# Performance work log

Measured on AMD Instinct MI355X. Metric: run time of the kernel, lower is better.

## Reference

```python
import jax, jax.numpy as jnp
import numpy as np

N_NODES = 100000
N_EDGES = 1600000
D_IN = 128
D_HID = 128
D_OUT = 64


def setup_inputs() -> dict:
    key = jax.random.key(0)
    ks = jax.random.split(key, 8)
    x = jax.random.normal(ks[0], (N_NODES, D_IN), dtype=jnp.float32)
    edge_index = jax.random.randint(ks[1], (2, N_EDGES), 0, N_NODES, dtype=jnp.int64)
    s = 1.0 / np.sqrt(D_IN)
    W1l = jax.random.uniform(ks[2], (D_IN, D_HID), minval=-s, maxval=s, dtype=jnp.float32)
    W1r = jax.random.uniform(ks[3], (D_IN, D_HID), minval=-s, maxval=s, dtype=jnp.float32)
    b1 = jnp.zeros((D_HID,), dtype=jnp.float32)
    s2 = 1.0 / np.sqrt(D_HID)
    W2l = jax.random.uniform(ks[4], (D_HID, D_OUT), minval=-s2, maxval=s2, dtype=jnp.float32)
    W2r = jax.random.uniform(ks[5], (D_HID, D_OUT), minval=-s2, maxval=s2, dtype=jnp.float32)
    b2 = jnp.zeros((D_OUT,), dtype=jnp.float32)
    return {"x": x, "edge_index": edge_index, "drpt": 0,
            "W1l": W1l, "W1r": W1r, "b1": b1,
            "W2l": W2l, "W2r": W2r, "b2": b2}


def _mean_aggregate(x, src, dst, n_nodes):
    # gather source features along edges, scatter-mean to destinations
    gathered = x[src]                                   # [E, d]
    summed = jax.ops.segment_sum(gathered, dst, num_segments=n_nodes)  # [N, d]
    deg = jax.ops.segment_sum(jnp.ones((src.shape[0],), x.dtype), dst,
                              num_segments=n_nodes)     # [N]
    return summed / jnp.maximum(deg, 1.0)[:, None]


def _sage_conv(x, src, dst, Wl, Wr, b):
    # PyG SAGEConv (mean): out = agg @ Wl + b + x @ Wr
    agg = _mean_aggregate(x, src, dst, x.shape[0])
    return agg @ Wl + b + x @ Wr


def reference(x, edge_index, drpt, W1l, W1r, b1, W2l, W2r, b2):
    src, dst = edge_index[0], edge_index[1]
    h = _sage_conv(x, src, dst, W1l, W1r, b1)
    h = jax.nn.relu(h)
    # dropout is identity at inference (training=False)
    out = _sage_conv(h, src, dst, W2l, W2r, b2)
    return out
```

## Files before the change

kernel.cpp:

```cpp
#include <hip/hip_runtime.h>
#include <hip/hip_bf16.h>


#define N_NODES 100000
#define NGRP 6250
#define NBKT 391
#define ECHUNK 8192
#define BCAP 12288
#define NXB 12500
#define NWB 192

typedef __attribute__((ext_vector_type(8))) short short8v;
typedef __attribute__((ext_vector_type(4))) float f32x4;
typedef __attribute__((ext_vector_type(2))) uint u32x2;

__device__ inline ushort bf16_rne(float f) {
    union { float f; uint u; } c; c.f = f;
    uint u = c.u;
    return (ushort)((u + 0x7FFFu + ((u >> 16) & 1u)) >> 16);
}
__device__ inline float bf16_f(ushort h) {
    union { uint u; float f; } c; c.u = (uint)h << 16;
    return c.f;
}
__device__ inline unsigned char fp8_enc(float f) {
    union { float f; uint u; } c; c.f = f;
    uint u = c.u;
    uint s = (u >> 24) & 0x80u;
    uint a = u & 0x7FFFFFFFu;
    uint code;
    if (a >= 0x3C800000u) {
        uint r = a + 0x7FFFFu + ((a >> 20) & 1u);
        int e = (int)(r >> 23) - 120;
        uint mm = (r >> 20) & 7u;
        code = ((uint)e << 3) | mm;
        if (code > 0x7Eu) code = 0x7Eu;
    } else {
        code = (uint)(__uint_as_float(a) * 512.0f + 0.5f);
    }
    return (unsigned char)(s | code);
}

__device__ inline void gl_lds16(const void* g, void* l) {
    __builtin_amdgcn_global_load_lds(
        (const __attribute__((address_space(1))) uint*)g,
        (__attribute__((address_space(3))) uint*)l, 16, 0, 0);
}
__device__ inline uint lds_off(const void* p) {
    return (uint)(size_t)(const __attribute__((address_space(3))) char*)p;
}

__global__ __launch_bounds__(256) void k_prep(const float* __restrict__ x,
                                              const float* __restrict__ W1l,
                                              const float* __restrict__ W1r,
                                              const float* __restrict__ W2l,
                                              const float* __restrict__ W2r,
                                              const int* __restrict__ dst, int E,
                                              ushort* __restrict__ xh,
                                              unsigned char* __restrict__ xf8,
                                              ushort* __restrict__ BT1h,
                                              ushort* __restrict__ BT1l,
                                              ushort* __restrict__ BT2h,
                                              ushort* __restrict__ BT2l,
                                              int* __restrict__ bhist) {
    __shared__ int hsh[NBKT];
    const int b = blockIdx.x;
    if (b < NXB) {
        int i = (b * 256 + threadIdx.x) * 4;
        float4 v = *(const float4*)&x[i];
        ushort4 hh;
        hh.x = bf16_rne(v.x); hh.y = bf16_rne(v.y);
        hh.z = bf16_rne(v.z); hh.w = bf16_rne(v.w);
        *(ushort4*)&xh[i] = hh;
        uint f8 = (uint)fp8_enc(v.x) | ((uint)fp8_enc(v.y) << 8) |
                  ((uint)fp8_enc(v.z) << 16) | ((uint)fp8_enc(v.w) << 24);
        *(uint*)&xf8[i] = f8;
    } else if (b < NXB + NWB) {
        int id = (b - NXB) * 256 + threadIdx.x;
        if (id < 32768) {
            int n = id >> 8, k = id & 255;
            float v = (k < 128) ? W1l[k * 128 + n] : W1r[(k - 128) * 128 + n];
            ushort h = bf16_rne(v);
            BT1h[id] = h;
            BT1l[id] = bf16_rne(v - bf16_f(h));
        } else {
            int i = id - 32768;
            int n = i >> 7, k = i & 127;
            float v = (n < 64) ? W2l[k * 64 + n] : W2r[k * 64 + (n - 64)];
            ushort h = bf16_rne(v);
            BT2h[i] = h;
            BT2l[i] = bf16_rne(v - bf16_f(h));
        }
    } else {
        int bb = b - NXB - NWB;
        for (int i = threadIdx.x; i < NBKT; i += 256) hsh[i] = 0;
        __syncthreads();
        int b0 = bb * ECHUNK;
        for (int i = threadIdx.x; i < ECHUNK; i += 256) {
            int e = b0 + i;
            if (e < E) atomicAdd(&hsh[dst[e] >> 8], 1);
        }
        __syncthreads();
        for (int i = threadIdx.x; i < NBKT; i += 256)
            if (hsh[i]) atomicAdd(&bhist[i], hsh[i]);
    }
}

__global__ __launch_bounds__(512) void kA2_scan(const int* __restrict__ bhist,
                                                int* __restrict__ boff,
                                                int* __restrict__ bcur) {
    __shared__ int s[512];
    int t = threadIdx.x;
    s[t] = (t < NBKT) ? bhist[t] : 0;
    __syncthreads();
    for (int d = 1; d < 512; d <<= 1) {
        int v = (t >= d) ? s[t - d] : 0;
        __syncthreads();
        s[t] += v;
        __syncthreads();
    }
    if (t <= NBKT) {
        int e = (t == 0) ? 0 : s[t - 1];
        boff[t] = e;
        if (t < NBKT) bcur[t] = e;
    }
}

__global__ __launch_bounds__(256) void kA3_scatter(const int* __restrict__ src,
                                                   const int* __restrict__ dst,
                                                   int* __restrict__ bcur,
                                                   int* __restrict__ pairs, int E) {
    __shared__ int hist[NBKT];
    __shared__ int base[NBKT];
    __shared__ ushort rank[ECHUNK];
    for (int i = threadIdx.x; i < NBKT; i += 256) hist[i] = 0;
    __syncthreads();
    int b0 = blockIdx.x * ECHUNK;
    for (int i = threadIdx.x; i < ECHUNK; i += 256) {
        int e = b0 + i;
        if (e < E) rank[i] = (ushort)atomicAdd(&hist[dst[e] >> 8], 1);
    }
    __syncthreads();
    for (int i = threadIdx.x; i < NBKT; i += 256) {
        int c = hist[i];
        base[i] = c ? atomicAdd(&bcur[i], c) : 0;
    }
    __syncthreads();
    for (int i = threadIdx.x; i < ECHUNK; i += 256) {
        int e = b0 + i;
        if (e < E) {
            int d = dst[e];
            pairs[base[d >> 8] + rank[i]] = src[e] | ((d & 255) << 17);
        }
    }
}

__global__ __launch_bounds__(256) void kB_build(const int* __restrict__ pairs,
                                                const int* __restrict__ boff,
                                                int* __restrict__ csr,
                                                unsigned char* __restrict__ ldst,
                                                int* __restrict__ offsets,
                                                float* __restrict__ invdeg,
                                                int N, int E) {
    __shared__ int cntk[256];
    __shared__ int sck[256];
    __shared__ int cur[256];
    __shared__ int cntn[256];
    __shared__ int stage[BCAP];
    const int b = blockIdx.x;
    const int gbase = boff[b], gcount = boff[b + 1] - gbase;
    const int n0 = b << 8;
    const int t = threadIdx.x;

    cntk[t] = 0; cntn[t] = 0;
    __syncthreads();
    for (int i = t; i < gcount; i += 256) {
        int p = pairs[gbase + i];
        int dlow = (p >> 17) & 255;
        int key = (dlow & 0xF0) | ((p & 0x1FFFF) >> 13);
        atomicAdd(&cntk[key], 1);
        atomicAdd(&cntn[dlow], 1);
    }
    __syncthreads();
    sck[t] = cntk[t];
    __syncthreads();
    for (int d = 1; d < 256; d <<= 1) {
        int v = (t >= d) ? sck[t - d] : 0;
        __syncthreads();
        sck[t] += v;
        __syncthreads();
    }
    cur[t] = sck[t] - cntk[t];
    int node = n0 + t;
    if (node < N) {
        int gk = t & 0xF0;
        offsets[node] = gbase + sck[gk] - cntk[gk];
        invdeg[node] = 1.0f / fmaxf((float)cntn[t], 1.0f);
    }
    if (b == NBKT - 1 && t == 0) offsets[N] = E;
    __syncthreads();

    if (gcount <= BCAP) {
        for (int i = t; i < gcount; i += 256) {
            int p = pairs[gbase + i];
            int key = ((p >> 17) & 0xF0) | ((p & 0x1FFFF) >> 13);
            int pos = atomicAdd(&cur[key], 1);
            stage[pos] = p;
        }
        __syncthreads();
        for (int i = t; i < gcount; i += 256) {
            int p = stage[i];
            csr[gbase + i] = p & 0x1FFFF;
            ldst[gbase + i] = (unsigned char)((p >> 17) & 15);
        }
    } else {
        for (int i = t; i < gcount; i += 256) {
            int p = pairs[gbase + i];
            int key = ((p >> 17) & 0xF0) | ((p & 0x1FFFF) >> 13);
            int pos = atomicAdd(&cur[key], 1);
            csr[gbase + pos] = p & 0x1FFFF;
            ldst[gbase + pos] = (unsigned char)((p >> 17) & 15);
        }
    }
}

__global__ __launch_bounds__(256, 8) void k_agg1(const unsigned char* __restrict__ xf8,
                                                 const int* __restrict__ csr,
                                                 const unsigned char* __restrict__ ldst,
                                                 const int* __restrict__ off,
                                                 const float* __restrict__ invdeg,
                                                 ushort* __restrict__ ah, int E) {
    __shared__ char smem[16384];
    const int wv = threadIdx.x >> 6, lane = threadIdx.x & 63;
    const int g = blockIdx.x * 4 + wv;
    if (g >= NGRP) return;
    const int gbase = off[g * 16], gend = off[g * 16 + 16];
    const int cnt = gend - gbase;
    const int m = lane & 15;
    const int e_meta = lane & 31;
    const int t_hi = lane >> 5;
    const int Emax = E - 1;
    char* stg = smem + wv * 4096;

    f32x4 acc[8] = {};
    const int nch = (cnt + 31) >> 5;

    int pe = gbase + e_meta;
    int se = csr[(pe < Emax) ? pe : Emax];
    int lb = (pe < gend) ? (int)ldst[pe] : 255;

    for (int ch = 0; ch < nch; ++ch) {
        const char* rowbase = (const char*)xf8 + (size_t)se * 128;
        #pragma unroll
        for (int c = 0; c < 4; ++c)
            gl_lds16(rowbase + (c * 2 + t_hi) * 16, stg + c * 1024);

        int p = gbase + (ch + 1) * 32 + e_meta;
        se = csr[(p < Emax) ? p : Emax];
        int lbn = (p < gend) ? (int)ldst[p] : 255;

        asm volatile("s_waitcnt vmcnt(0)" ::: "memory");
        __builtin_amdgcn_sched_barrier(0);

        unsigned long long av = 0ull;
        #pragma unroll
        for (int j = 0; j < 8; ++j) {
            int k = (lane >> 4) * 8 + j;
            int b = __shfl(lb, k);
            av |= (b == m) ? (0x38ull << (8 * j)) : 0ull;
        }

        uint base0 = lds_off(stg) + lane * 8;
        #pragma unroll
        for (int th = 0; th < 2; ++th) {
            u32x2 tb[4];
            #pragma unroll
            for (int t = 0; t < 4; ++t) {
                uint a1 = base0 + (th * 4 + t) * 512;
                asm volatile("ds_read_b64_tr_b8 %0, %1" : "=v"(tb[t]) : "v"(a1));
            }
            asm volatile("s_waitcnt lgkmcnt(0)" ::: "memory");
            __builtin_amdgcn_sched_barrier(0);
            #pragma unroll
            for (int t = 0; t < 4; ++t) {
                unsigned long long bv = ((unsigned long long)tb[t].y << 32) | tb[t].x;
                acc[th * 4 + t] = __builtin_amdgcn_mfma_f32_16x16x32_fp8_fp8(
                    (long long)av, (long long)bv, acc[th * 4 + t], 0, 0, 0);
            }
            __builtin_amdgcn_sched_barrier(0);
        }
        lb = lbn;
    }

    float idv[4];
    #pragma unroll
    for (int i = 0; i < 4; ++i) idv[i] = invdeg[g * 16 + (lane >> 4) * 4 + i];
    #pragma unroll
    for (int t = 0; t < 8; ++t) {
        #pragma unroll
        for (int i = 0; i < 4; ++i) {
            int node = g * 16 + (lane >> 4) * 4 + i;
            ah[(size_t)node * 128 + t * 16 + m] = bf16_rne(acc[t][i] * idv[i]);
        }
    }
}

__global__ __launch_bounds__(256, 8) void k_agg2(const ushort* __restrict__ hWl,
                                                 const float* __restrict__ hWr,
                                                 const int* __restrict__ csr,
                                                 const unsigned char* __restrict__ ldst,
                                                 const int* __restrict__ off,
                                                 const float* __restrict__ invdeg,
                                                 const float* __restrict__ b2,
                                                 float* __restrict__ out, int E) {
    __shared__ char smem[16384];
    const int wv = threadIdx.x >> 6, lane = threadIdx.x & 63;
    const int g = blockIdx.x * 4 + wv;
    if (g >= NGRP) return;
    const int gbase = off[g * 16], gend = off[g * 16 + 16];
    const int cnt = gend - gbase;
    const int m = lane & 15;
    const int phys = lane >> 3;
    const int E4 = (phys < 4) ? phys * 2 : (phys - 4) * 2 + 1;
    const int e_st = E4 * 4 + ((lane >> 1) & 3);
    const int e_meta = lane & 31;
    const int Emax = E - 1;
    char* stg = smem + wv * 4096;

    f32x4 acc[4] = {};
    const int nch = (cnt + 31) >> 5;

    int ps = gbase + e_st;
    int se = csr[(ps < Emax) ? ps : Emax];
    int pm = gbase + e_meta;
    int lb = (pm < gend) ? (int)ldst[pm] : 255;

    for (int ch = 0; ch < nch; ++ch) {
        const char* gsrc = (const char*)hWl + (size_t)se * 128 + (lane & 1) * 16;
        #pragma unroll
        for (int c = 0; c < 4; ++c)
            gl_lds16(gsrc + c * 32, stg + c * 1024);

        int p = gbase + (ch + 1) * 32;
        int ps2 = p + e_st;
        se = csr[(ps2 < Emax) ? ps2 : Emax];
        int pm2 = p + e_meta;
        int lbn = (pm2 < gend) ? (int)ldst[pm2] : 255;

        asm volatile("s_waitcnt vmcnt(0)" ::: "memory");
        __builtin_amdgcn_sched_barrier(0);

        uint au[4];
        #pragma unroll
        for (int jp = 0; jp < 4; ++jp) {
            int k0 = (lane >> 4) * 8 + jp * 2;
            int b0 = __shfl(lb, k0);
            int b1 = __shfl(lb, k0 + 1);
            au[jp] = ((b0 == m) ? 0x3F80u : 0u) | (((b1 == m) ? 0x3F80u : 0u) << 16);
        }
        union { uint u[4]; short8v v; } A_;
        A_.u[0] = au[0]; A_.u[1] = au[1]; A_.u[2] = au[2]; A_.u[3] = au[3];

        uint base0 = lds_off(stg) + lane * 8;
        #pragma unroll
        for (int th = 0; th < 2; ++th) {
            u32x2 t1[2], t2[2];
            #pragma unroll
            for (int t = 0; t < 2; ++t) {
                uint a1 = base0 + (th * 2 + t) * 1024;
                uint a2 = a1 + 512;
                asm volatile("ds_read_b64_tr_b16 %0, %1" : "=v"(t1[t]) : "v"(a1));
                asm volatile("ds_read_b64_tr_b16 %0, %1" : "=v"(t2[t]) : "v"(a2));
            }
            asm volatile("s_waitcnt lgkmcnt(0)" ::: "memory");
            __builtin_amdgcn_sched_barrier(0);
            #pragma unroll
            for (int t = 0; t < 2; ++t) {
                union { uint u[4]; short8v v; } B_;
                B_.u[0] = t1[t].x; B_.u[1] = t1[t].y;
                B_.u[2] = t2[t].x; B_.u[3] = t2[t].y;
                acc[th * 2 + t] = __builtin_amdgcn_mfma_f32_16x16x32_bf16(
                    A_.v, B_.v, acc[th * 2 + t], 0, 0, 0);
            }
            __builtin_amdgcn_sched_barrier(0);
        }
        lb = lbn;
    }

    float idv[4];
    #pragma unroll
    for (int i = 0; i < 4; ++i) idv[i] = invdeg[g * 16 + (lane >> 4) * 4 + i];
    #pragma unroll
    for (int t = 0; t < 4; ++t) {
        #pragma unroll
        for (int i = 0; i < 4; ++i) {
            int node = g * 16 + (lane >> 4) * 4 + i;
            size_t idx = (size_t)node * 64 + t * 16 + m;
            out[idx] = acc[t][i] * idv[i] + hWr[idx] + b2[t * 16 + m];
        }
    }
}

__global__ __launch_bounds__(256) void k_mfma12(
    const ushort* __restrict__ Agg, const ushort* __restrict__ X,
    const ushort* __restrict__ B1h, const ushort* __restrict__ B1l,
    const ushort* __restrict__ B2h, const ushort* __restrict__ B2l,
    const float* __restrict__ b1,
    ushort* __restrict__ hWl, float* __restrict__ hWr, int M) {
    __shared__ ushort Ah[128 * 40], Bh[128 * 40], Bl[128 * 40];
    __shared__ ushort hT[4 * 128 * 40];

    const int tid = threadIdx.x;
    const int wid = tid >> 6, lane = tid & 63;
    const int wm = wid >> 1, wn = wid & 1;
    const int m0 = blockIdx.x * 128;
    const int rl = lane & 15, kof = (lane >> 4) * 8;
    const int rq = lane >> 4;

    const int r0 = tid >> 2, r1 = (tid + 256) >> 2;
    const int cq = tid & 3;
    int g0 = m0 + r0; if (g0 >= M) g0 = M - 1;
    int g1 = m0 + r1; if (g1 >= M) g1 = M - 1;
    const int ldso0 = r0 * 40 + cq * 8;
    const int ldso1 = r1 * 40 + cq * 8;

    short8v pA0, pA1, pB0, pB1, pL0, pL1;
    {
        int gk = cq * 8;
        pA0 = *(const short8v*)&Agg[(size_t)g0 * 128 + gk];
        pA1 = *(const short8v*)&Agg[(size_t)g1 * 128 + gk];
        pB0 = *(const short8v*)&B1h[r0 * 256 + gk];
        pB1 = *(const short8v*)&B1h[r1 * 256 + gk];
        pL0 = *(const short8v*)&B1l[r0 * 256 + gk];
        pL1 = *(const short8v*)&B1l[r1 * 256 + gk];
    }
    f32x4 acc[4][4] = {};
    for (int kc = 0; kc < 8; ++kc) {
        *(short8v*)&Ah[ldso0] = pA0; *(short8v*)&Ah[ldso1] = pA1;
        *(short8v*)&Bh[ldso0] = pB0; *(short8v*)&Bh[ldso1] = pB1;
        *(short8v*)&Bl[ldso0] = pL0; *(short8v*)&Bl[ldso1] = pL1;
        __syncthreads();

        if (kc < 7) {
            int gk = (kc + 1) * 32 + cq * 8;
            const ushort* s0 = (gk >= 128) ? &X[(size_t)g0 * 128 + gk - 128]
                                           : &Agg[(size_t)g0 * 128 + gk];
            const ushort* s1 = (gk >= 128) ? &X[(size_t)g1 * 128 + gk - 128]
                                           : &Agg[(size_t)g1 * 128 + gk];
            pA0 = *(const short8v*)s0;
            pA1 = *(const short8v*)s1;
            pB0 = *(const short8v*)&B1h[r0 * 256 + gk];
            pB1 = *(const short8v*)&B1h[r1 * 256 + gk];
            pL0 = *(const short8v*)&B1l[r0 * 256 + gk];
            pL1 = *(const short8v*)&B1l[r1 * 256 + gk];
        }

        short8v a_h[4], b_h[4], b_l[4];
        #pragma unroll
        for (int f = 0; f < 4; ++f) {
            int ra = wm * 64 + f * 16 + rl;
            int rb = wn * 64 + f * 16 + rl;
            a_h[f] = *(const short8v*)&Ah[ra * 40 + kof];
            b_h[f] = *(const short8v*)&Bh[rb * 40 + kof];
            b_l[f] = *(const short8v*)&Bl[rb * 40 + kof];
        }
        #pragma unroll
        for (int mf = 0; mf < 4; ++mf)
            #pragma unroll
            for (int nf = 0; nf < 4; ++nf) {
                acc[mf][nf] = __builtin_amdgcn_mfma_f32_16x16x32_bf16(a_h[mf], b_h[nf], acc[mf][nf], 0, 0, 0);
                acc[mf][nf] = __builtin_amdgcn_mfma_f32_16x16x32_bf16(a_h[mf], b_l[nf], acc[mf][nf], 0, 0, 0);
            }
        __syncthreads();
    }

    short8v qB0, qB1, qL0, qL1;
    {
        int gk = cq * 8;
        qB0 = *(const short8v*)&B2h[r0 * 128 + gk];
        qB1 = *(const short8v*)&B2h[r1 * 128 + gk];
        qL0 = *(const short8v*)&B2l[r0 * 128 + gk];
        qL1 = *(const short8v*)&B2l[r1 * 128 + gk];
    }

    #pragma unroll
    for (int mf = 0; mf < 4; ++mf)
        #pragma unroll
        for (int nf = 0; nf < 4; ++nf) {
            int col = wn * 64 + nf * 16 + rl;
            float bv = b1[col];
            #pragma unroll
            for (int i = 0; i < 4; ++i) {
                int rloc = wm * 64 + mf * 16 + rq * 4 + i;
                float v = fmaxf(acc[mf][nf][i] + bv, 0.0f);
                hT[((col >> 5) * 128 + rloc) * 40 + (col & 31)] = bf16_rne(v);
            }
        }
    __syncthreads();

    f32x4 acc2[4][4] = {};
    for (int kc = 0; kc < 4; ++kc) {
        *(short8v*)&Bh[ldso0] = qB0; *(short8v*)&Bh[ldso1] = qB1;
        *(short8v*)&Bl[ldso0] = qL0; *(short8v*)&Bl[ldso1] = qL1;
        __syncthreads();

        if (kc < 3) {
            int gk = (kc + 1) * 32 + cq * 8;
            qB0 = *(const short8v*)&B2h[r0 * 128 + gk];
            qB1 = *(const short8v*)&B2h[r1 * 128 + gk];
            qL0 = *(const short8v*)&B2l[r0 * 128 + gk];
            qL1 = *(const short8v*)&B2l[r1 * 128 + gk];
        }

        short8v a_h[4], b_h[4], b_l[4];
        #pragma unroll
        for (int f = 0; f < 4; ++f) {
            int ra = wm * 64 + f * 16 + rl;
            int rb = wn * 64 + f * 16 + rl;
            a_h[f] = *(const short8v*)&hT[(kc * 128 + ra) * 40 + kof];
            b_h[f] = *(const short8v*)&Bh[rb * 40 + kof];
            b_l[f] = *(const short8v*)&Bl[rb * 40 + kof];
        }
        #pragma unroll
        for (int mf = 0; mf < 4; ++mf)
            #pragma unroll
            for (int nf = 0; nf < 4; ++nf) {
                acc2[mf][nf] = __builtin_amdgcn_mfma_f32_16x16x32_bf16(a_h[mf], b_h[nf], acc2[mf][nf], 0, 0, 0);
                acc2[mf][nf] = __builtin_amdgcn_mfma_f32_16x16x32_bf16(a_h[mf], b_l[nf], acc2[mf][nf], 0, 0, 0);
            }
        __syncthreads();
    }

    #pragma unroll
    for (int mf = 0; mf < 4; ++mf)
        #pragma unroll
        for (int nf = 0; nf < 4; ++nf) {
            int col = wn * 64 + nf * 16 + rl;
            #pragma unroll
            for (int i = 0; i < 4; ++i) {
                int row = m0 + wm * 64 + mf * 16 + rq * 4 + i;
                if (row < M) {
                    float v = acc2[mf][nf][i];
                    if (col < 64) hWl[(size_t)row * 64 + col] = bf16_rne(v);
                    else          hWr[(size_t)row * 64 + col - 64] = v;
                }
            }
        }
}

extern "C" void kernel_launch(void* const* d_in, const int* in_sizes, int n_in,
                              void* d_out, int out_size, void* d_ws, size_t ws_size,
                              hipStream_t stream) {
    const float* x   = (const float*)d_in[0];
    const int*   ei  = (const int*)d_in[1];
    const float* W1l = (const float*)d_in[3];
    const float* W1r = (const float*)d_in[4];
    const float* b1  = (const float*)d_in[5];
    const float* W2l = (const float*)d_in[6];
    const float* W2r = (const float*)d_in[7];
    const float* b2  = (const float*)d_in[8];
    float* out = (float*)d_out;

    const int N = N_NODES;
    const int E = in_sizes[1] / 2;
    const int* src = ei;
    const int* dst = ei + E;
    const int NEB = (E + ECHUNK - 1) / ECHUNK;

    char* ws = (char*)d_ws;
    int*           bhist   = (int*)   (ws + 0);
    int*           boff    = (int*)   (ws + 4096);
    int*           bcur    = (int*)   (ws + 8192);
    int*           offsets = (int*)   (ws + 12288);
    float*         invdeg  = (float*) (ws + 417792);
    int*           csr     = (int*)   (ws + 819200);
    unsigned char* ldst    = (unsigned char*)(ws + 7220224);
    unsigned char* x_f8    = (unsigned char*)(ws + 8821760);
    ushort*        x_hi    = (ushort*)(ws + 21622784);
    ushort*        agg_hi  = (ushort*)(ws + 47223808);
    float*         hWr     = (float*) (ws + 98425856);
    ushort*        BT1h    = (ushort*)(ws + 124026880);
    ushort*        BT1l    = (ushort*)(ws + 124092416);
    ushort*        BT2h    = (ushort*)(ws + 124157952);
    ushort*        BT2l    = (ushort*)(ws + 124190720);
    int*           pairs   = (int*)   (ws + 98425856);
    ushort*        hWl     = (ushort*)(ws + 72824832);

    hipMemsetAsync(bhist, 0, NBKT * 4, stream);

    k_prep<<<NXB + NWB + NEB, 256, 0, stream>>>(x, W1l, W1r, W2l, W2r, dst, E,
                                                x_hi, x_f8, BT1h, BT1l, BT2h, BT2l, bhist);
    kA2_scan<<<1, 512, 0, stream>>>(bhist, boff, bcur);
    kA3_scatter<<<NEB, 256, 0, stream>>>(src, dst, bcur, pairs, E);
    kB_build<<<NBKT, 256, 0, stream>>>(pairs, boff, csr, ldst, offsets, invdeg, N, E);

    const int GAGG = (NGRP + 3) / 4;
    k_agg1<<<GAGG, 256, 0, stream>>>(x_f8, csr, ldst, offsets, invdeg, agg_hi, E);

    const int MB = (N + 127) / 128;
    k_mfma12<<<MB, 256, 0, stream>>>(agg_hi, x_hi, BT1h, BT1l, BT2h, BT2l,
                                     b1, hWl, hWr, N);

    k_agg2<<<GAGG, 256, 0, stream>>>(hWl, hWr, csr, ldst, offsets, invdeg, b2, out, E);
}
```

Before: 195.8 us.

## Swizzle LDS staging layout and use single-wave blocks for aggregation kernels

Both aggregation kernels now launch one 64-thread wave per block with its own 4KB shared staging buffer, in place of four waves sharing a 256-thread block. The gather now has each 8-lane group fetch a whole 128-byte source row, with the row index taken by shuffle, which makes global reads contiguous per row. An XOR swizzle on the LDS column offset is matched in the transpose-read addresses, aiming to avoid bank conflicts. The risks are more, smaller blocks to schedule and extra shuffle instructions in the inner loop.

```diff
diff --git a/kernel.cpp b/kernel.cpp
--- a/kernel.cpp
+++ b/kernel.cpp
@@ -224,23 +224,22 @@
     }
 }
 
-__global__ __launch_bounds__(256, 8) void k_agg1(const unsigned char* __restrict__ xf8,
-                                                 const int* __restrict__ csr,
-                                                 const unsigned char* __restrict__ ldst,
-                                                 const int* __restrict__ off,
-                                                 const float* __restrict__ invdeg,
-                                                 ushort* __restrict__ ah, int E) {
-    __shared__ char smem[16384];
-    const int wv = threadIdx.x >> 6, lane = threadIdx.x & 63;
-    const int g = blockIdx.x * 4 + wv;
-    if (g >= NGRP) return;
+__global__ __launch_bounds__(64, 8) void k_agg1(const unsigned char* __restrict__ xf8,
+                                                const int* __restrict__ csr,
+                                                const unsigned char* __restrict__ ldst,
+                                                const int* __restrict__ off,
+                                                const float* __restrict__ invdeg,
+                                                ushort* __restrict__ ah, int E) {
+    __shared__ __align__(1024) char stg[4096];
+    const int lane = threadIdx.x;
+    const int g = blockIdx.x;
     const int gbase = off[g * 16], gend = off[g * 16 + 16];
     const int cnt = gend - gbase;
     const int m = lane & 15;
     const int e_meta = lane & 31;
-    const int t_hi = lane >> 5;
     const int Emax = E - 1;
-    char* stg = smem + wv * 4096;
+    const int esrc = lane >> 3;
+    const int koff = ((lane & 7) ^ (esrc & 7)) << 4;
 
     f32x4 acc[8] = {};
     const int nch = (cnt + 31) >> 5;
@@ -249,11 +248,15 @@
     int se = csr[(pe < Emax) ? pe : Emax];
     int lb = (pe < gend) ? (int)ldst[pe] : 255;
 
+    const uint e7 = (lane >> 1) & 7;
+    const uint bbase = lds_off(stg) + (uint)((lane >> 1) * 128 + (lane & 1) * 8);
+
     for (int ch = 0; ch < nch; ++ch) {
-        const char* rowbase = (const char*)xf8 + (size_t)se * 128;
-        #pragma unroll
-        for (int c = 0; c < 4; ++c)
-            gl_lds16(rowbase + (c * 2 + t_hi) * 16, stg + c * 1024);
+        #pragma unroll
+        for (int c = 0; c < 4; ++c) {
+            int rs = __shfl(se, c * 8 + esrc);
+            gl_lds16((const char*)xf8 + (size_t)rs * 128 + koff, stg + c * 1024);
+        }
 
         int p = gbase + (ch + 1) * 32 + e_meta;
         se = csr[(p < Emax) ? p : Emax];
@@ -270,22 +273,22 @@
             av |= (b == m) ? (0x38ull << (8 * j)) : 0ull;
         }
 
-        uint base0 = lds_off(stg) + lane * 8;
         #pragma unroll
         for (int th = 0; th < 2; ++th) {
             u32x2 tb[4];
             #pragma unroll
-            for (int t = 0; t < 4; ++t) {
-                uint a1 = base0 + (th * 4 + t) * 512;
-                asm volatile("ds_read_b64_tr_b8 %0, %1" : "=v"(tb[t]) : "v"(a1));
+            for (int t4 = 0; t4 < 4; ++t4) {
+                uint t = (uint)(th * 4 + t4);
+                uint a1 = bbase + ((t ^ e7) << 4);
+                asm volatile("ds_read_b64_tr_b8 %0, %1" : "=v"(tb[t4]) : "v"(a1));
             }
             asm volatile("s_waitcnt lgkmcnt(0)" ::: "memory");
             __builtin_amdgcn_sched_barrier(0);
             #pragma unroll
-            for (int t = 0; t < 4; ++t) {
-                unsigned long long bv = ((unsigned long long)tb[t].y << 32) | tb[t].x;
-                acc[th * 4 + t] = __builtin_amdgcn_mfma_f32_16x16x32_fp8_fp8(
-                    (long long)av, (long long)bv, acc[th * 4 + t], 0, 0, 0);
+            for (int t4 = 0; t4 < 4; ++t4) {
+                unsigned long long bv = ((unsigned long long)tb[t4].y << 32) | tb[t4].x;
+                acc[th * 4 + t4] = __builtin_amdgcn_mfma_f32_16x16x32_fp8_fp8(
+                    (long long)av, (long long)bv, acc[th * 4 + t4], 0, 0, 0);
             }
             __builtin_amdgcn_sched_barrier(0);
         }
@@ -305,47 +308,46 @@
     }
 }
 
-__global__ __launch_bounds__(256, 8) void k_agg2(const ushort* __restrict__ hWl,
-                                                 const float* __restrict__ hWr,
-                                                 const int* __restrict__ csr,
-                                                 const unsigned char* __restrict__ ldst,
-                                                 const int* __restrict__ off,
-                                                 const float* __restrict__ invdeg,
-                                                 const float* __restrict__ b2,
-                                                 float* __restrict__ out, int E) {
-    __shared__ char smem[16384];
-    const int wv = threadIdx.x >> 6, lane = threadIdx.x & 63;
-    const int g = blockIdx.x * 4 + wv;
-    if (g >= NGRP) return;
+__global__ __launch_bounds__(64, 8) void k_agg2(const ushort* __restrict__ hWl,
+                                                const float* __restrict__ hWr,
+                                                const int* __restrict__ csr,
+                                                const unsigned char* __restrict__ ldst,
+                                                const int* __restrict__ off,
+                                                const float* __restrict__ invdeg,
+                                                const float* __restrict__ b2,
+                                                float* __restrict__ out, int E) {
+    __shared__ __align__(1024) char stg[4096];
+    const int lane = threadIdx.x;
+    const int g = blockIdx.x;
     const int gbase = off[g * 16], gend = off[g * 16 + 16];
     const int cnt = gend - gbase;
     const int m = lane & 15;
-    const int phys = lane >> 3;
-    const int E4 = (phys < 4) ? phys * 2 : (phys - 4) * 2 + 1;
-    const int e_st = E4 * 4 + ((lane >> 1) & 3);
     const int e_meta = lane & 31;
     const int Emax = E - 1;
-    char* stg = smem + wv * 4096;
+    const int esrc = lane >> 3;
+    const int koff = ((lane & 7) ^ ((esrc & 3) << 1)) << 4;
 
     f32x4 acc[4] = {};
     const int nch = (cnt + 31) >> 5;
 
-    int ps = gbase + e_st;
-    int se = csr[(ps < Emax) ? ps : Emax];
-    int pm = gbase + e_meta;
-    int lb = (pm < gend) ? (int)ldst[pm] : 255;
+    int pe = gbase + e_meta;
+    int se = csr[(pe < Emax) ? pe : Emax];
+    int lb = (pe < gend) ? (int)ldst[pe] : 255;
+
+    const uint he = ((lane >> 1) & 1) ^ (((lane >> 2) & 3) << 1);
+    const uint bbase = lds_off(stg) +
+        (uint)(((lane >> 4) * 8 + ((lane >> 2) & 3)) * 128 + (lane & 1) * 8);
 
     for (int ch = 0; ch < nch; ++ch) {
-        const char* gsrc = (const char*)hWl + (size_t)se * 128 + (lane & 1) * 16;
-        #pragma unroll
-        for (int c = 0; c < 4; ++c)
-            gl_lds16(gsrc + c * 32, stg + c * 1024);
-
-        int p = gbase + (ch + 1) * 32;
-        int ps2 = p + e_st;
-        se = csr[(ps2 < Emax) ? ps2 : Emax];
-        int pm2 = p + e_meta;
-        int lbn = (pm2 < gend) ? (int)ldst[pm2] : 255;
+        #pragma unroll
+        for (int c = 0; c < 4; ++c) {
+            int rs = __shfl(se, c * 8 + esrc);
+            gl_lds16((const char*)hWl + (size_t)rs * 128 + koff, stg + c * 1024);
+        }
+
+        int p = gbase + (ch + 1) * 32 + e_meta;
+        se = csr[(p < Emax) ? p : Emax];
+        int lbn = (p < gend) ? (int)ldst[p] : 255;
 
         asm volatile("s_waitcnt vmcnt(0)" ::: "memory");
         __builtin_amdgcn_sched_barrier(0);
@@ -361,26 +363,27 @@
         union { uint u[4]; short8v v; } A_;
         A_.u[0] = au[0]; A_.u[1] = au[1]; A_.u[2] = au[2]; A_.u[3] = au[3];
 
-        uint base0 = lds_off(stg) + lane * 8;
         #pragma unroll
         for (int th = 0; th < 2; ++th) {
             u32x2 t1[2], t2[2];
             #pragma unroll
-            for (int t = 0; t < 2; ++t) {
-                uint a1 = base0 + (th * 2 + t) * 1024;
+            for (int tt = 0; tt < 2; ++tt) {
+                uint t = (uint)(th * 2 + tt);
+                uint seg = (2u * t) ^ he;
+                uint a1 = bbase + (seg << 4);
                 uint a2 = a1 + 512;
-                asm volatile("ds_read_b64_tr_b16 %0, %1" : "=v"(t1[t]) : "v"(a1));
-                asm volatile("ds_read_b64_tr_b16 %0, %1" : "=v"(t2[t]) : "v"(a2));
+                asm volatile("ds_read_b64_tr_b16 %0, %1" : "=v"(t1[tt]) : "v"(a1));
+                asm volatile("ds_read_b64_tr_b16 %0, %1" : "=v"(t2[tt]) : "v"(a2));
             }
             asm volatile("s_waitcnt lgkmcnt(0)" ::: "memory");
             __builtin_amdgcn_sched_barrier(0);
             #pragma unroll
-            for (int t = 0; t < 2; ++t) {
+            for (int tt = 0; tt < 2; ++tt) {
                 union { uint u[4]; short8v v; } B_;
-                B_.u[0] = t1[t].x; B_.u[1] = t1[t].y;
-                B_.u[2] = t2[t].x; B_.u[3] = t2[t].y;
-                acc[th * 2 + t] = __builtin_amdgcn_mfma_f32_16x16x32_bf16(
-                    A_.v, B_.v, acc[th * 2 + t], 0, 0, 0);
+                B_.u[0] = t1[tt].x; B_.u[1] = t1[tt].y;
+                B_.u[2] = t2[tt].x; B_.u[3] = t2[tt].y;
+                acc[th * 2 + tt] = __builtin_amdgcn_mfma_f32_16x16x32_bf16(
+                    A_.v, B_.v, acc[th * 2 + tt], 0, 0, 0);
             }
             __builtin_amdgcn_sched_barrier(0);
         }
@@ -594,12 +597,11 @@
     kA3_scatter<<<NEB, 256, 0, stream>>>(src, dst, bcur, pairs, E);
     kB_build<<<NBKT, 256, 0, stream>>>(pairs, boff, csr, ldst, offsets, invdeg, N, E);
 
-    const int GAGG = (NGRP + 3) / 4;
-    k_agg1<<<GAGG, 256, 0, stream>>>(x_f8, csr, ldst, offsets, invdeg, agg_hi, E);
+    k_agg1<<<NGRP, 64, 0, stream>>>(x_f8, csr, ldst, offsets, invdeg, agg_hi, E);
 
     const int MB = (N + 127) / 128;
     k_mfma12<<<MB, 256, 0, stream>>>(agg_hi, x_hi, BT1h, BT1l, BT2h, BT2l,
                                      b1, hWl, hWr, N);
 
-    k_agg2<<<GAGG, 256, 0, stream>>>(hWl, hWr, csr, ldst, offsets, invdeg, b2, out, E);
-}
+    k_agg2<<<NGRP, 64, 0, stream>>>(hWl, hWr, csr, ldst, offsets, invdeg, b2, out, E);
+}
```

New measurement: 173.6 us. -11.3%, faster.
